# Kernel optimization log

Hardware: AMD Instinct MI355X
Metric: run time of the kernel (lower is better)

The kernel has to match this reference:

```python
import jax, jax.numpy as jnp
import numpy as np

L, N, D = 2, 100000, 128
TRACE_HID, MVC_DIM, MVC_HID = 256, 128, 64
NUM_EDGE = 1600000
TAU = 0.5


def setup_inputs() -> dict:
    key = jax.random.key(0)
    ks = jax.random.split(key, 9)
    trace_all = jax.random.normal(ks[0], (L, N, D), dtype=jnp.float32)
    W_lin = jax.random.normal(ks[1], (TRACE_HID, L * D), dtype=jnp.float32) * 0.05
    W_lin2 = jax.random.normal(ks[2], (MVC_DIM, TRACE_HID), dtype=jnp.float32) * 0.05
    W_fc1 = jax.random.normal(ks[3], (MVC_HID, 2 * MVC_DIM), dtype=jnp.float32) * 0.05
    b_fc1 = jax.random.normal(ks[4], (MVC_HID,), dtype=jnp.float32) * 0.05
    W_fc2 = jax.random.normal(ks[5], (2, MVC_HID), dtype=jnp.float32) * 0.05
    b_fc2 = jax.random.normal(ks[6], (2,), dtype=jnp.float32) * 0.05
    u = jax.random.uniform(ks[7], (NUM_EDGE, 2), dtype=jnp.float32, minval=1e-6, maxval=1.0 - 1e-6)
    gumbel = -jnp.log(-jnp.log(u))  # standard Gumbel(0,1) noise
    edge_index = jax.random.randint(ks[8], (2, 3 * NUM_EDGE), 0, N, dtype=jnp.int32)
    return {
        "trace_all": trace_all, "W_lin": W_lin, "W_lin2": W_lin2,
        "W_fc1": W_fc1, "b_fc1": b_fc1, "W_fc2": W_fc2, "b_fc2": b_fc2,
        "gumbel": gumbel, "edge_index": edge_index, "num_edge": NUM_EDGE,
    }


def reference(trace_all, W_lin, W_lin2, W_fc1, b_fc1, W_fc2, b_fc2, gumbel, edge_index, num_edge):
    # --- TraceMLP: [L, N, d] -> mvc [N, mvc_dim] (eval mode: dropout is identity)
    l, n, d = trace_all.shape
    x = jnp.transpose(trace_all, (1, 0, 2)).reshape(n, l * d)      # [N, L*d]
    h = jax.nn.relu(x @ W_lin.T)                                   # [N, trace_hidden]
    mvc = h @ W_lin2.T                                             # [N, mvc_dim]
    norm = jnp.maximum(jnp.linalg.norm(mvc, axis=1, keepdims=True), 1e-12)
    mvc = mvc / norm                                               # F.normalize(p=2, dim=1)

    # --- EdgeScoringNet over non-slow edges (first num_edge columns)
    src = edge_index[0, :num_edge]
    dst = edge_index[1, :num_edge]
    comb = jnp.concatenate([mvc[src], mvc[dst]], axis=1)           # [E, 2*mvc_dim]
    h2 = jax.nn.relu(comb @ W_fc1.T + b_fc1)                       # [E, mvc_hidden]
    scores = h2 @ W_fc2.T + b_fc2                                  # [E, 2]

    # --- gumbel_softmax(tau=0.5, hard=True)[:, 0] (straight-through)
    y_soft = jax.nn.softmax((scores + gumbel) / TAU, axis=-1)
    y_hard = jax.nn.one_hot(jnp.argmax(y_soft, axis=-1), 2, dtype=y_soft.dtype)
    ret = y_hard - jax.lax.stop_gradient(y_soft) + y_soft
    active = ret[:, 0]                                             # [E], values in {0,1}

    # --- train_mask: first block = active, next two blocks = 1 - active
    train_mask = jnp.concatenate([active, 1.0 - active, 1.0 - active])  # [3*E]
    return train_mask
```

## Files before the change

kernel.cpp:

```cpp
#include <hip/hip_runtime.h>

#define NN   100000
#define EE   1600000
#define EROW 4800000

typedef _Float16 half8 __attribute__((ext_vector_type(8)));
typedef float    f32x4 __attribute__((ext_vector_type(4)));

__device__ __forceinline__ float4 ld4(const float* p){ return *(const float4*)p; }

__device__ __forceinline__ unsigned splitf(float v) {
    _Float16 h = (_Float16)v;
    float r = v - (float)h;
    _Float16 l = (_Float16)(r * 2048.0f);
    union { _Float16 f; unsigned short u; } uh, ul;
    uh.f = h; ul.f = l;
    return (unsigned)uh.u | ((unsigned)ul.u << 16);
}

__global__ __launch_bounds__(256)
void prep_w(const float* __restrict__ W1, const float* __restrict__ W2,
            const float* __restrict__ W3, unsigned* __restrict__ o1,
            unsigned* __restrict__ o2, unsigned* __restrict__ o3)
{
    int idx = blockIdx.x * 256 + threadIdx.x;
    if (idx < 65536) {
        o1[idx] = splitf(W1[idx]);
    } else if (idx < 98304) {
        int i = idx - 65536;
        o2[i] = splitf(W2[i]);
    } else {
        int i = idx - 98304;
        int j = i >> 7, k = i & 127;
        o3[i] = splitf(W3[(j & 63) * 256 + (j >> 6) * 128 + k]);
    }
}

template<int SRCA, int EPI>
__global__ __launch_bounds__(256, 2)
void gemm_mfma(const void* __restrict__ Asrc, const unsigned* __restrict__ Bw,
               const float* __restrict__ bias, unsigned* __restrict__ outS,
               float* __restrict__ outF, int M, int K, int No)
{
    __shared__ __align__(16) _Float16 Ah[128][40];
    __shared__ __align__(16) _Float16 Al[128][40];
    __shared__ __align__(16) _Float16 Bh[128][40];
    __shared__ __align__(16) _Float16 Bl[128][40];
    __shared__ float sq[128][2];

    const int t     = threadIdx.x;
    const int wm    = (t >> 6) >> 1;
    const int wn    = (t >> 6) & 1;
    const int lane  = t & 63;
    const int lm    = lane & 15;
    const int q     = lane >> 4;
    const int mBase = blockIdx.x * 128;
    const int nBase = blockIdx.y * 128;

    const int srow = t >> 3;
    const int sseg = (t & 7) * 4;

    f32x4 aH[4][4], aM[4][4];
#pragma unroll
    for (int i = 0; i < 4; ++i)
#pragma unroll
        for (int j = 0; j < 4; ++j) {
            aH[i][j] = (f32x4){0.f, 0.f, 0.f, 0.f};
            aM[i][j] = (f32x4){0.f, 0.f, 0.f, 0.f};
        }

    uint2 sAh[4], sAl[4], sBh[4], sBl[4];

    auto loadStage = [&](int k0) {
#pragma unroll
        for (int it = 0; it < 4; ++it) {
            const int row = srow + it * 32;
            int rg = mBase + row; rg = rg < M ? rg : M - 1;
            if (SRCA == 0) {
                const int k = k0 + sseg;
                const float* ap = (const float*)Asrc
                    + (size_t)(k >> 7) * ((size_t)NN * 128)
                    + (size_t)rg * 128 + (k & 127);
                float4 f = ld4(ap);
                unsigned p0 = splitf(f.x), p1 = splitf(f.y);
                unsigned p2 = splitf(f.z), p3 = splitf(f.w);
                sAh[it].x = (p0 & 0xffffu) | (p1 << 16);
                sAh[it].y = (p2 & 0xffffu) | (p3 << 16);
                sAl[it].x = (p0 >> 16) | (p1 & 0xffff0000u);
                sAl[it].y = (p2 >> 16) | (p3 & 0xffff0000u);
            } else {
                const unsigned* ap = (const unsigned*)Asrc + (size_t)rg * K + k0 + sseg;
                uint4 u = *(const uint4*)ap;
                sAh[it].x = (u.x & 0xffffu) | (u.y << 16);
                sAh[it].y = (u.z & 0xffffu) | (u.w << 16);
                sAl[it].x = (u.x >> 16) | (u.y & 0xffff0000u);
                sAl[it].y = (u.z >> 16) | (u.w & 0xffff0000u);
            }
            const unsigned* bp = Bw + (size_t)(nBase + row) * K + k0 + sseg;
            uint4 ub = *(const uint4*)bp;
            sBh[it].x = (ub.x & 0xffffu) | (ub.y << 16);
            sBh[it].y = (ub.z & 0xffffu) | (ub.w << 16);
            sBl[it].x = (ub.x >> 16) | (ub.y & 0xffff0000u);
            sBl[it].y = (ub.z >> 16) | (ub.w & 0xffff0000u);
        }
    };

    loadStage(0);
    const int nk = K / 32;
    for (int kt = 0; kt < nk; ++kt) {
        __syncthreads();
#pragma unroll
        for (int it = 0; it < 4; ++it) {
            const int row = srow + it * 32;
            *(uint2*)&Ah[row][sseg] = sAh[it];
            *(uint2*)&Al[row][sseg] = sAl[it];
            *(uint2*)&Bh[row][sseg] = sBh[it];
            *(uint2*)&Bl[row][sseg] = sBl[it];
        }
        __syncthreads();
        if (kt + 1 < nk) loadStage((kt + 1) * 32);

        half8 fAh[4], fAl[4], fBh[4], fBl[4];
#pragma unroll
        for (int i = 0; i < 4; ++i) {
            fAh[i] = *(const half8*)&Ah[wm * 64 + i * 16 + lm][q * 8];
            fAl[i] = *(const half8*)&Al[wm * 64 + i * 16 + lm][q * 8];
            fBh[i] = *(const half8*)&Bh[wn * 64 + i * 16 + lm][q * 8];
            fBl[i] = *(const half8*)&Bl[wn * 64 + i * 16 + lm][q * 8];
        }
#pragma unroll
        for (int i = 0; i < 4; ++i)
#pragma unroll
            for (int j = 0; j < 4; ++j)
                aH[i][j] = __builtin_amdgcn_mfma_f32_16x16x32_f16(fAh[i], fBh[j], aH[i][j], 0, 0, 0);
#pragma unroll
        for (int i = 0; i < 4; ++i)
#pragma unroll
            for (int j = 0; j < 4; ++j)
                aM[i][j] = __builtin_amdgcn_mfma_f32_16x16x32_f16(fAh[i], fBl[j], aM[i][j], 0, 0, 0);
#pragma unroll
        for (int i = 0; i < 4; ++i)
#pragma unroll
            for (int j = 0; j < 4; ++j)
                aM[i][j] = __builtin_amdgcn_mfma_f32_16x16x32_f16(fAl[i], fBh[j], aM[i][j], 0, 0, 0);
    }

    const float cM = 1.0f / 2048.0f;
#pragma unroll
    for (int i = 0; i < 4; ++i)
#pragma unroll
        for (int j = 0; j < 4; ++j)
            aH[i][j] = aH[i][j] + aM[i][j] * cM;

    float nm[4][4];
    if (EPI == 1) {
#pragma unroll
        for (int i = 0; i < 4; ++i)
#pragma unroll
            for (int r = 0; r < 4; ++r) {
                float s = 0.f;
#pragma unroll
                for (int j = 0; j < 4; ++j) { float x = aH[i][j][r]; s = fmaf(x, x, s); }
#pragma unroll
                for (int off = 1; off < 16; off <<= 1) s += __shfl_xor(s, off, 16);
                if (lm == 0) sq[wm * 64 + i * 16 + q * 4 + r][wn] = s;
            }
        __syncthreads();
#pragma unroll
        for (int i = 0; i < 4; ++i)
#pragma unroll
            for (int r = 0; r < 4; ++r) {
                const int rl = wm * 64 + i * 16 + q * 4 + r;
                nm[i][r] = fmaxf(sqrtf(sq[rl][0] + sq[rl][1]), 1e-12f);
            }
    }

    float bj[4] = {0.f, 0.f, 0.f, 0.f};
    if (EPI == 2 && wn == 0) {
#pragma unroll
        for (int j = 0; j < 4; ++j) bj[j] = bias[j * 16 + lm];
    }

#pragma unroll
    for (int i = 0; i < 4; ++i)
#pragma unroll
        for (int r = 0; r < 4; ++r) {
            const int m = mBase + wm * 64 + i * 16 + q * 4 + r;
            if (m < M) {
#pragma unroll
                for (int j = 0; j < 4; ++j) {
                    const int c = nBase + wn * 64 + j * 16 + lm;
                    float v = aH[i][j][r];
                    if (EPI == 0) { v = fmaxf(v, 0.f); outS[(size_t)m * No + c] = splitf(v); }
                    if (EPI == 1) { v = v / nm[i][r];  outS[(size_t)m * No + c] = splitf(v); }
                    if (EPI == 2) { v += bj[j];        outF[(size_t)m * No + c] = v; }
                }
            }
        }
}

#define EPB 128
__global__ __launch_bounds__(256, 4)
void edge_k(const float* __restrict__ p, const int* __restrict__ ei,
            const float* __restrict__ gum, const float* __restrict__ W2,
            const float* __restrict__ b2, float* __restrict__ out)
{
    __shared__ int   sidx[EPB];
    __shared__ int   didx[EPB];
    __shared__ float gl[2 * EPB];
    __shared__ float act[EPB];

    const int t  = threadIdx.x;
    const int e0 = blockIdx.x * EPB;

    if (t < EPB) sidx[t] = ei[e0 + t];
    else         didx[t - EPB] = ei[EROW + e0 + (t - EPB)];
    gl[t] = gum[(size_t)e0 * 2 + t];
    __syncthreads();

    const int j   = t & 15;
    const int grp = t >> 4;
    const float4 w0 = ld4(&W2[j * 4]);
    const float4 w1 = ld4(&W2[64 + j * 4]);
    const float b20 = b2[0], b21 = b2[1];

    float4 pa[8], pb[8];
#pragma unroll
    for (int it = 0; it < 8; ++it) {
        const int el = grp * 8 + it;
        pa[it] = ld4(&p[(size_t)sidx[el] * 128 + j * 4]);
        pb[it] = ld4(&p[(size_t)didx[el] * 128 + 64 + j * 4]);
    }

#pragma unroll
    for (int it = 0; it < 8; ++it) {
        const int el = grp * 8 + it;
        const float r0 = fmaxf(pa[it].x + pb[it].x, 0.f);
        const float r1 = fmaxf(pa[it].y + pb[it].y, 0.f);
        const float r2 = fmaxf(pa[it].z + pb[it].z, 0.f);
        const float r3 = fmaxf(pa[it].w + pb[it].w, 0.f);
        float s0 = r0 * w0.x + r1 * w0.y + r2 * w0.z + r3 * w0.w;
        float s1 = r0 * w1.x + r1 * w1.y + r2 * w1.z + r3 * w1.w;
#pragma unroll
        for (int off = 1; off < 16; off <<= 1) {
            s0 += __shfl_xor(s0, off, 16);
            s1 += __shfl_xor(s1, off, 16);
        }
        if (j == 0) {
            const float sc0 = s0 + b20 + gl[el * 2];
            const float sc1 = s1 + b21 + gl[el * 2 + 1];
            act[el] = (sc0 >= sc1) ? 1.f : 0.f;
        }
    }
    __syncthreads();

    if (t < EPB) {
        const float a = act[t];
        const size_t e = (size_t)e0 + t;
        out[e]                  = a;
        out[EE + e]             = 1.f - a;
        out[2 * (size_t)EE + e] = 1.f - a;
    }
}

extern "C" void kernel_launch(void* const* d_in, const int* in_sizes, int n_in,
                              void* d_out, int out_size, void* d_ws, size_t ws_size,
                              hipStream_t stream)
{
    const float* trace  = (const float*)d_in[0];
    const float* W_lin  = (const float*)d_in[1];
    const float* W_lin2 = (const float*)d_in[2];
    const float* W_fc1  = (const float*)d_in[3];
    const float* b_fc1  = (const float*)d_in[4];
    const float* W_fc2  = (const float*)d_in[5];
    const float* b_fc2  = (const float*)d_in[6];
    const float* gum    = (const float*)d_in[7];
    const int*   ei     = (const int*)  d_in[8];
    float*       out    = (float*)d_out;

    char* ws = (char*)d_ws;
    unsigned* hpl  = (unsigned*)ws;
    unsigned* mpl  = (unsigned*)(ws + (size_t)NN * 256 * 4);
    unsigned* W1i  = (unsigned*)(ws + (size_t)NN * 256 * 4 + (size_t)NN * 128 * 4);
    unsigned* W2i  = W1i + 65536;
    unsigned* W3i  = W2i + 32768;
    float*    p    = (float*)ws;

    prep_w<<<448, 256, 0, stream>>>(W_lin, W_lin2, W_fc1, W1i, W2i, W3i);

    const int mB = (NN + 127) / 128;

    gemm_mfma<0, 0><<<dim3(mB, 2), 256, 0, stream>>>(trace, W1i, nullptr, hpl, nullptr, NN, 256, 256);
    gemm_mfma<1, 1><<<dim3(mB, 1), 256, 0, stream>>>(hpl, W2i, nullptr, mpl, nullptr, NN, 256, 128);
    gemm_mfma<1, 2><<<dim3(mB, 1), 256, 0, stream>>>(mpl, W3i, b_fc1, nullptr, p, NN, 128, 128);
    edge_k<<<EE / EPB, 256, 0, stream>>>(p, ei, gum, W_fc2, b_fc2, out);
}
```

Before: 417.0 us.

## Gather fp16 node projections in edge kernel with fp32 fallback near ties

The GEMM epilogue now writes an fp16 copy of the per-node fc1 projections next to the fp32 one. The edge kernel gathers the half-width rows and computes a score gap plus an error bound. It reloads the fp32 rows only when the gap is within that bound, so most edges read half the gather bytes while near-ties keep exact decisions. Separately, the GEMM shared tiles are double-buffered to drop one barrier per k-step, at the cost of twice the LDS and possibly lower occupancy.

Result: faster. 371.6 us (-10.9%).

```diff
diff --git a/kernel.cpp b/kernel.cpp
--- a/kernel.cpp
+++ b/kernel.cpp
@@ -5,6 +5,7 @@
 #define EROW 4800000
 
 typedef _Float16 half8 __attribute__((ext_vector_type(8)));
+typedef _Float16 half4 __attribute__((ext_vector_type(4)));
 typedef float    f32x4 __attribute__((ext_vector_type(4)));
 
 __device__ __forceinline__ float4 ld4(const float* p){ return *(const float4*)p; }
@@ -40,13 +41,14 @@
 __global__ __launch_bounds__(256, 2)
 void gemm_mfma(const void* __restrict__ Asrc, const unsigned* __restrict__ Bw,
                const float* __restrict__ bias, unsigned* __restrict__ outS,
-               float* __restrict__ outF, int M, int K, int No)
+               float* __restrict__ outF, unsigned short* __restrict__ outH,
+               int M, int K, int No)
 {
-    __shared__ __align__(16) _Float16 Ah[128][40];
-    __shared__ __align__(16) _Float16 Al[128][40];
-    __shared__ __align__(16) _Float16 Bh[128][40];
-    __shared__ __align__(16) _Float16 Bl[128][40];
-    __shared__ float sq[128][2];
+    __shared__ __align__(16) _Float16 Ah[2][128][40];
+    __shared__ __align__(16) _Float16 Al[2][128][40];
+    __shared__ __align__(16) _Float16 Bh[2][128][40];
+    __shared__ __align__(16) _Float16 Bl[2][128][40];
+    float* sqv = (float*)&Ah[0][0][0];
 
     const int t     = threadIdx.x;
     const int wm    = (t >> 6) >> 1;
@@ -108,14 +110,14 @@
     loadStage(0);
     const int nk = K / 32;
     for (int kt = 0; kt < nk; ++kt) {
-        __syncthreads();
+        const int b = kt & 1;
 #pragma unroll
         for (int it = 0; it < 4; ++it) {
             const int row = srow + it * 32;
-            *(uint2*)&Ah[row][sseg] = sAh[it];
-            *(uint2*)&Al[row][sseg] = sAl[it];
-            *(uint2*)&Bh[row][sseg] = sBh[it];
-            *(uint2*)&Bl[row][sseg] = sBl[it];
+            *(uint2*)&Ah[b][row][sseg] = sAh[it];
+            *(uint2*)&Al[b][row][sseg] = sAl[it];
+            *(uint2*)&Bh[b][row][sseg] = sBh[it];
+            *(uint2*)&Bl[b][row][sseg] = sBl[it];
         }
         __syncthreads();
         if (kt + 1 < nk) loadStage((kt + 1) * 32);
@@ -123,10 +125,10 @@
         half8 fAh[4], fAl[4], fBh[4], fBl[4];
 #pragma unroll
         for (int i = 0; i < 4; ++i) {
-            fAh[i] = *(const half8*)&Ah[wm * 64 + i * 16 + lm][q * 8];
-            fAl[i] = *(const half8*)&Al[wm * 64 + i * 16 + lm][q * 8];
-            fBh[i] = *(const half8*)&Bh[wn * 64 + i * 16 + lm][q * 8];
-            fBl[i] = *(const half8*)&Bl[wn * 64 + i * 16 + lm][q * 8];
+            fAh[i] = *(const half8*)&Ah[b][wm * 64 + i * 16 + lm][q * 8];
+            fAl[i] = *(const half8*)&Al[b][wm * 64 + i * 16 + lm][q * 8];
+            fBh[i] = *(const half8*)&Bh[b][wn * 64 + i * 16 + lm][q * 8];
+            fBl[i] = *(const half8*)&Bl[b][wn * 64 + i * 16 + lm][q * 8];
         }
 #pragma unroll
         for (int i = 0; i < 4; ++i)
@@ -154,6 +156,7 @@
 
     float nm[4][4];
     if (EPI == 1) {
+        __syncthreads();
 #pragma unroll
         for (int i = 0; i < 4; ++i)
 #pragma unroll
@@ -163,7 +166,7 @@
                 for (int j = 0; j < 4; ++j) { float x = aH[i][j][r]; s = fmaf(x, x, s); }
 #pragma unroll
                 for (int off = 1; off < 16; off <<= 1) s += __shfl_xor(s, off, 16);
-                if (lm == 0) sq[wm * 64 + i * 16 + q * 4 + r][wn] = s;
+                if (lm == 0) sqv[(wm * 64 + i * 16 + q * 4 + r) * 2 + wn] = s;
             }
         __syncthreads();
 #pragma unroll
@@ -171,7 +174,7 @@
 #pragma unroll
             for (int r = 0; r < 4; ++r) {
                 const int rl = wm * 64 + i * 16 + q * 4 + r;
-                nm[i][r] = fmaxf(sqrtf(sq[rl][0] + sq[rl][1]), 1e-12f);
+                nm[i][r] = fmaxf(sqrtf(sqv[rl * 2] + sqv[rl * 2 + 1]), 1e-12f);
             }
     }
 
@@ -193,7 +196,12 @@
                     float v = aH[i][j][r];
                     if (EPI == 0) { v = fmaxf(v, 0.f); outS[(size_t)m * No + c] = splitf(v); }
                     if (EPI == 1) { v = v / nm[i][r];  outS[(size_t)m * No + c] = splitf(v); }
-                    if (EPI == 2) { v += bj[j];        outF[(size_t)m * No + c] = v; }
+                    if (EPI == 2) {
+                        v += bj[j];
+                        outF[(size_t)m * No + c] = v;
+                        union { _Float16 f; unsigned short u; } cv; cv.f = (_Float16)v;
+                        outH[(size_t)m * No + c] = cv.u;
+                    }
                 }
             }
         }
@@ -201,9 +209,10 @@
 
 #define EPB 128
 __global__ __launch_bounds__(256, 4)
-void edge_k(const float* __restrict__ p, const int* __restrict__ ei,
-            const float* __restrict__ gum, const float* __restrict__ W2,
-            const float* __restrict__ b2, float* __restrict__ out)
+void edge_k(const unsigned short* __restrict__ pH, const float* __restrict__ p,
+            const int* __restrict__ ei, const float* __restrict__ gum,
+            const float* __restrict__ W2, const float* __restrict__ b2,
+            float* __restrict__ out)
 {
     __shared__ int   sidx[EPB];
     __shared__ int   didx[EPB];
@@ -222,35 +231,64 @@
     const int grp = t >> 4;
     const float4 w0 = ld4(&W2[j * 4]);
     const float4 w1 = ld4(&W2[64 + j * 4]);
+    const float4 dw = make_float4(fabsf(w0.x - w1.x), fabsf(w0.y - w1.y),
+                                  fabsf(w0.z - w1.z), fabsf(w0.w - w1.w));
     const float b20 = b2[0], b21 = b2[1];
 
-    float4 pa[8], pb[8];
+    union U8 { uint2 u; half4 h; };
+    U8 ua[8], ub[8];
 #pragma unroll
     for (int it = 0; it < 8; ++it) {
         const int el = grp * 8 + it;
-        pa[it] = ld4(&p[(size_t)sidx[el] * 128 + j * 4]);
-        pb[it] = ld4(&p[(size_t)didx[el] * 128 + 64 + j * 4]);
+        ua[it].u = *(const uint2*)&pH[(size_t)sidx[el] * 128 + j * 4];
+        ub[it].u = *(const uint2*)&pH[(size_t)didx[el] * 128 + 64 + j * 4];
     }
 
 #pragma unroll
     for (int it = 0; it < 8; ++it) {
         const int el = grp * 8 + it;
-        const float r0 = fmaxf(pa[it].x + pb[it].x, 0.f);
-        const float r1 = fmaxf(pa[it].y + pb[it].y, 0.f);
-        const float r2 = fmaxf(pa[it].z + pb[it].z, 0.f);
-        const float r3 = fmaxf(pa[it].w + pb[it].w, 0.f);
+        const float a0 = (float)ua[it].h[0], a1 = (float)ua[it].h[1];
+        const float a2 = (float)ua[it].h[2], a3 = (float)ua[it].h[3];
+        const float c0 = (float)ub[it].h[0], c1 = (float)ub[it].h[1];
+        const float c2 = (float)ub[it].h[2], c3 = (float)ub[it].h[3];
+        const float r0 = fmaxf(a0 + c0, 0.f);
+        const float r1 = fmaxf(a1 + c1, 0.f);
+        const float r2 = fmaxf(a2 + c2, 0.f);
+        const float r3 = fmaxf(a3 + c3, 0.f);
         float s0 = r0 * w0.x + r1 * w0.y + r2 * w0.z + r3 * w0.w;
         float s1 = r0 * w1.x + r1 * w1.y + r2 * w1.z + r3 * w1.w;
+        float eb = dw.x * (fabsf(a0) + fabsf(c0)) + dw.y * (fabsf(a1) + fabsf(c1))
+                 + dw.z * (fabsf(a2) + fabsf(c2)) + dw.w * (fabsf(a3) + fabsf(c3));
 #pragma unroll
         for (int off = 1; off < 16; off <<= 1) {
             s0 += __shfl_xor(s0, off, 16);
             s1 += __shfl_xor(s1, off, 16);
-        }
-        if (j == 0) {
-            const float sc0 = s0 + b20 + gl[el * 2];
-            const float sc1 = s1 + b21 + gl[el * 2 + 1];
-            act[el] = (sc0 >= sc1) ? 1.f : 0.f;
-        }
+            eb += __shfl_xor(eb, off, 16);
+        }
+        const float g0 = gl[el * 2], g1 = gl[el * 2 + 1];
+        const float gap = (s0 + b20 + g0) - (s1 + b21 + g1);
+        const float bound = eb * 0.0009765625f + 2e-5f;
+        float av;
+        if (fabsf(gap) > bound) {
+            av = (gap >= 0.f) ? 1.f : 0.f;
+        } else {
+            const float4 pa = ld4(&p[(size_t)sidx[el] * 128 + j * 4]);
+            const float4 pb = ld4(&p[(size_t)didx[el] * 128 + 64 + j * 4]);
+            const float q0 = fmaxf(pa.x + pb.x, 0.f);
+            const float q1 = fmaxf(pa.y + pb.y, 0.f);
+            const float q2 = fmaxf(pa.z + pb.z, 0.f);
+            const float q3 = fmaxf(pa.w + pb.w, 0.f);
+            float t0 = q0 * w0.x + q1 * w0.y + q2 * w0.z + q3 * w0.w;
+            float t1 = q0 * w1.x + q1 * w1.y + q2 * w1.z + q3 * w1.w;
+#pragma unroll
+            for (int off = 1; off < 16; off <<= 1) {
+                t0 += __shfl_xor(t0, off, 16);
+                t1 += __shfl_xor(t1, off, 16);
+            }
+            const float ge = (t0 + b20 + g0) - (t1 + b21 + g1);
+            av = (ge >= 0.f) ? 1.f : 0.f;
+        }
+        if (j == 0) act[el] = av;
     }
     __syncthreads();
 
@@ -279,19 +317,20 @@
     float*       out    = (float*)d_out;
 
     char* ws = (char*)d_ws;
-    unsigned* hpl  = (unsigned*)ws;
-    unsigned* mpl  = (unsigned*)(ws + (size_t)NN * 256 * 4);
-    unsigned* W1i  = (unsigned*)(ws + (size_t)NN * 256 * 4 + (size_t)NN * 128 * 4);
-    unsigned* W2i  = W1i + 65536;
-    unsigned* W3i  = W2i + 32768;
-    float*    p    = (float*)ws;
+    unsigned*       hpl = (unsigned*)ws;
+    unsigned*       mpl = (unsigned*)(ws + (size_t)NN * 256 * 4);
+    unsigned*       W1i = (unsigned*)(ws + (size_t)NN * 256 * 4 + (size_t)NN * 128 * 4);
+    unsigned*       W2i = W1i + 65536;
+    unsigned*       W3i = W2i + 32768;
+    float*          p   = (float*)ws;
+    unsigned short* pH  = (unsigned short*)(ws + (size_t)NN * 128 * 4);
 
     prep_w<<<448, 256, 0, stream>>>(W_lin, W_lin2, W_fc1, W1i, W2i, W3i);
 
     const int mB = (NN + 127) / 128;
 
-    gemm_mfma<0, 0><<<dim3(mB, 2), 256, 0, stream>>>(trace, W1i, nullptr, hpl, nullptr, NN, 256, 256);
-    gemm_mfma<1, 1><<<dim3(mB, 1), 256, 0, stream>>>(hpl, W2i, nullptr, mpl, nullptr, NN, 256, 128);
-    gemm_mfma<1, 2><<<dim3(mB, 1), 256, 0, stream>>>(mpl, W3i, b_fc1, nullptr, p, NN, 128, 128);
-    edge_k<<<EE / EPB, 256, 0, stream>>>(p, ei, gum, W_fc2, b_fc2, out);
-}
+    gemm_mfma<0, 0><<<dim3(mB, 2), 256, 0, stream>>>(trace, W1i, nullptr, hpl, nullptr, nullptr, NN, 256, 256);
+    gemm_mfma<1, 1><<<dim3(mB, 1), 256, 0, stream>>>(hpl, W2i, nullptr, mpl, nullptr, nullptr, NN, 256, 128);
+    gemm_mfma<1, 2><<<dim3(mB, 1), 256, 0, stream>>>(mpl, W3i, b_fc1, nullptr, p, pH, NN, 128, 128);
+    edge_k<<<EE / EPB, 256, 0, stream>>>(pH, p, ei, gum, W_fc2, b_fc2, out);
+}
```
